# Kernel tuning notes

Measured on AMD Instinct MI355X. Metric: run time of the kernel, lower is better.

## Reference

```python
import jax, jax.numpy as jnp
import numpy as np

N_NODES = 100000


def spmm(edge_src, edge_dst, edge_val, x):
    """z[dst] += val * x[src] over all edges (COO sparse-dense matmul)."""
    gathered = edge_val[:, None] * x[edge_src]  # [E, d]
    return jax.ops.segment_sum(gathered, edge_dst, num_segments=N_NODES)


def setup_inputs() -> dict:
    key = jax.random.key(0)
    k1, k2, k3, k4, k5, k6 = jax.random.split(key, 6)
    N, E, IN, H, C = N_NODES, 1600000, 256, 128, 40
    features = jax.random.normal(k1, (N, IN), dtype=jnp.float32)
    # xavier_uniform-like init
    b1 = float(np.sqrt(6.0 / (IN + H)))
    b2 = float(np.sqrt(6.0 / (H + C)))
    W1 = jax.random.uniform(k2, (IN, H), dtype=jnp.float32, minval=-b1, maxval=b1)
    W2 = jax.random.uniform(k3, (H, C), dtype=jnp.float32, minval=-b2, maxval=b2)
    edge_src = jax.random.randint(k4, (E,), 0, N, dtype=jnp.int32)
    edge_dst = jnp.sort(jax.random.randint(k5, (E,), 0, N, dtype=jnp.int32))
    # normalized-adjacency-like positive edge weights
    edge_val = jax.random.uniform(k6, (E,), dtype=jnp.float32)
    return {"features": features, "W1": W1, "W2": W2,
            "edge_src": edge_src, "edge_dst": edge_dst, "edge_val": edge_val}


def reference(features, W1, W2, edge_src, edge_dst, edge_val):
    # Decoupled GCN: all dense NN layers first (relu between, none after last) ...
    h = jax.nn.relu(features @ W1)
    h = h @ W2  # [N, num_classes]
    # ... then nlayers (=2) rounds of graph propagation (spmm aggregation)
    h = spmm(edge_src, edge_dst, edge_val, h)
    h = spmm(edge_src, edge_dst, edge_val, h)
    return h
```

## Files before the change

kernel.cpp:

```cpp
#include <hip/hip_runtime.h>
#include <cstddef>
#include <cstdint>

#define IN_DIM 256
#define H_DIM  128
#define C_DIM  40
#define BM     128
#define BK     64
#define LDT    72
#define LDH    136
#define PAD_C  64

typedef short bf16x8 __attribute__((ext_vector_type(8)));
typedef float f32x16 __attribute__((ext_vector_type(16)));

__device__ __forceinline__ ushort f2bf(float f) {
  uint u = __builtin_bit_cast(uint, f);
  u += 0x7fffu + ((u >> 16) & 1u);
  return (ushort)(u >> 16);
}
__device__ __forceinline__ float bf2f(uint s) {
  uint u = s << 16;
  return __builtin_bit_cast(float, u);
}

__global__ void build_row_ptr_kernel(const int* __restrict__ dst, int E,
                                     int* __restrict__ row_ptr, int n1) {
  int n = blockIdx.x * blockDim.x + threadIdx.x;
  if (n >= n1) return;
  int lo = 0, hi = E;
  while (lo < hi) {
    int mid = (lo + hi) >> 1;
    if (dst[mid] < n) lo = mid + 1; else hi = mid;
  }
  row_ptr[n] = lo;
}

__global__ void convert_weights_kernel(const float* __restrict__ W1,
                                       const float* __restrict__ W2,
                                       ushort* __restrict__ w1t,
                                       ushort* __restrict__ w2t) {
  int tid = blockIdx.x * blockDim.x + threadIdx.x;
  if (tid < IN_DIM * H_DIM) {
    int k = tid >> 7, n = tid & 127;
    w1t[n * IN_DIM + k] = f2bf(W1[tid]);
  } else {
    int i = tid - IN_DIM * H_DIM;
    int n = i >> 7, k = i & 127;
    w2t[i] = (n < C_DIM) ? f2bf(W2[k * C_DIM + n]) : (ushort)0;
  }
}

__global__ __launch_bounds__(256, 3) void fused_dense_kernel(
    const float* __restrict__ feat, const ushort* __restrict__ w1t,
    const ushort* __restrict__ w2t, ushort* __restrict__ z0, int N) {
  __shared__ __align__(16) ushort smem[26112];

  const int t = threadIdx.x;
  const int w = t >> 6, l = t & 63;
  const int nb = blockIdx.x * BM;

  f32x16 acc[4];
#pragma unroll
  for (int tn = 0; tn < 4; ++tn)
#pragma unroll
    for (int r = 0; r < 16; ++r) acc[tn][r] = 0.f;

  const int srow = t >> 1;
  const int skh  = (t & 1) << 5;
  int grow = nb + srow; if (grow >= N) grow = N - 1;
  const float*  fp = feat + (size_t)grow * IN_DIM + skh;
  const ushort* wp = w1t + (srow << 8) + skh;

  const ushort* Abase = smem + (w * 32 + (l & 31)) * LDT + ((l >> 5) << 3);
  const ushort* Bbase = smem + 128 * LDT + (l & 31) * LDT + ((l >> 5) << 3);

  for (int kc = 0; kc < IN_DIM; kc += BK) {
    const float4* f4 = (const float4*)(fp + kc);
    uint* adst = (uint*)(smem + srow * LDT + skh);
#pragma unroll
    for (int i = 0; i < 4; ++i) {
      float4 v0 = f4[2 * i], v1 = f4[2 * i + 1];
      uint4 pk;
      pk.x = (uint)f2bf(v0.x) | ((uint)f2bf(v0.y) << 16);
      pk.y = (uint)f2bf(v0.z) | ((uint)f2bf(v0.w) << 16);
      pk.z = (uint)f2bf(v1.x) | ((uint)f2bf(v1.y) << 16);
      pk.w = (uint)f2bf(v1.z) | ((uint)f2bf(v1.w) << 16);
      ((uint4*)adst)[i] = pk;
    }
    const uint4* bsrc = (const uint4*)(wp + kc);
    uint4* bdst = (uint4*)(smem + 128 * LDT + srow * LDT + skh);
#pragma unroll
    for (int i = 0; i < 4; ++i) bdst[i] = bsrc[i];
    __syncthreads();

#pragma unroll
    for (int ks = 0; ks < 4; ++ks) {
      bf16x8 af = *(const bf16x8*)(Abase + ks * 16);
#pragma unroll
      for (int tn = 0; tn < 4; ++tn) {
        bf16x8 bfr = *(const bf16x8*)(Bbase + tn * 32 * LDT + ks * 16);
        acc[tn] = __builtin_amdgcn_mfma_f32_32x32x16_bf16(af, bfr, acc[tn], 0, 0, 0);
      }
    }
    __syncthreads();
  }

#pragma unroll
  for (int tn = 0; tn < 4; ++tn) {
    int col = tn * 32 + (l & 31);
#pragma unroll
    for (int r = 0; r < 16; ++r) {
      int nodeLoc = (r & 3) + 8 * (r >> 2) + 4 * (l >> 5) + 32 * w;
      float v = acc[tn][r];
      smem[nodeLoc * LDH + col] = f2bf(v > 0.f ? v : 0.f);
    }
  }
  {
    int row = t >> 2, c4 = (t & 3) << 5;
    const uint4* src = (const uint4*)(w2t + row * H_DIM + c4);
    uint4* dst = (uint4*)(smem + 128 * LDH + row * LDH + c4);
    dst[0] = src[0];
    dst[1] = src[1];
    dst[2] = src[2];
    dst[3] = src[3];
  }
  __syncthreads();

  f32x16 acc2[2];
#pragma unroll
  for (int tn = 0; tn < 2; ++tn)
#pragma unroll
    for (int r = 0; r < 16; ++r) acc2[tn][r] = 0.f;

  const ushort* Hbase  = smem + (w * 32 + (l & 31)) * LDH + ((l >> 5) << 3);
  const ushort* W2base = smem + 128 * LDH + (l & 31) * LDH + ((l >> 5) << 3);
#pragma unroll
  for (int kb = 0; kb < 8; ++kb) {
    bf16x8 af = *(const bf16x8*)(Hbase + kb * 16);
#pragma unroll
    for (int tn = 0; tn < 2; ++tn) {
      bf16x8 bfr = *(const bf16x8*)(W2base + tn * 32 * LDH + kb * 16);
      acc2[tn] = __builtin_amdgcn_mfma_f32_32x32x16_bf16(af, bfr, acc2[tn], 0, 0, 0);
    }
  }

#pragma unroll
  for (int tn = 0; tn < 2; ++tn) {
    int col = tn * 32 + (l & 31);
#pragma unroll
    for (int r = 0; r < 16; ++r) {
      int node = nb + 32 * w + (r & 3) + 8 * (r >> 2) + 4 * (l >> 5);
      if (node < N) z0[(size_t)node * PAD_C + col] = f2bf(acc2[tn][r]);
    }
  }
}

__global__ __launch_bounds__(256) void spmm_kernel(
    const int* __restrict__ row_ptr, const int* __restrict__ esrc,
    const float* __restrict__ eval, const ushort* __restrict__ x,
    ushort* __restrict__ zb, float* __restrict__ zf, int N, int out_f32) {
  int node = (blockIdx.x << 2) + (threadIdx.x >> 6);
  if (node >= N) return;
  const int lane = threadIdx.x & 63;
  const int h = lane >> 3;
  const int j = lane & 7;

  int e   = row_ptr[node];
  int end = row_ptr[node + 1];

  float acc[8];
#pragma unroll
  for (int c = 0; c < 8; ++c) acc[c] = 0.f;

  for (; e + 8 <= end; e += 8) {
    int   s = esrc[e + h];
    float v = eval[e + h];
    uint4 u = *(const uint4*)(x + (size_t)s * PAD_C + j * 8);
    acc[0] = fmaf(v, bf2f(u.x & 0xffffu), acc[0]);
    acc[1] = fmaf(v, bf2f(u.x >> 16),     acc[1]);
    acc[2] = fmaf(v, bf2f(u.y & 0xffffu), acc[2]);
    acc[3] = fmaf(v, bf2f(u.y >> 16),     acc[3]);
    acc[4] = fmaf(v, bf2f(u.z & 0xffffu), acc[4]);
    acc[5] = fmaf(v, bf2f(u.z >> 16),     acc[5]);
    acc[6] = fmaf(v, bf2f(u.w & 0xffffu), acc[6]);
    acc[7] = fmaf(v, bf2f(u.w >> 16),     acc[7]);
  }
  if (e < end) {
    int ei = e + h;
    int ec = ei < end - 1 ? ei : end - 1;
    int   s = esrc[ec];
    float v = (ei < end) ? eval[ec] : 0.f;
    uint4 u = *(const uint4*)(x + (size_t)s * PAD_C + j * 8);
    acc[0] = fmaf(v, bf2f(u.x & 0xffffu), acc[0]);
    acc[1] = fmaf(v, bf2f(u.x >> 16),     acc[1]);
    acc[2] = fmaf(v, bf2f(u.y & 0xffffu), acc[2]);
    acc[3] = fmaf(v, bf2f(u.y >> 16),     acc[3]);
    acc[4] = fmaf(v, bf2f(u.z & 0xffffu), acc[4]);
    acc[5] = fmaf(v, bf2f(u.z >> 16),     acc[5]);
    acc[6] = fmaf(v, bf2f(u.w & 0xffffu), acc[6]);
    acc[7] = fmaf(v, bf2f(u.w >> 16),     acc[7]);
  }

#pragma unroll
  for (int c = 0; c < 8; ++c) acc[c] += __shfl_xor(acc[c], 8);
#pragma unroll
  for (int c = 0; c < 8; ++c) acc[c] += __shfl_xor(acc[c], 16);
#pragma unroll
  for (int c = 0; c < 8; ++c) acc[c] += __shfl_xor(acc[c], 32);

  if (out_f32) {
    if (lane < 5) {
      float4 o0 = {acc[0], acc[1], acc[2], acc[3]};
      float4 o1 = {acc[4], acc[5], acc[6], acc[7]};
      float* p = zf + (size_t)node * C_DIM + j * 8;
      *(float4*)(p + 0) = o0;
      *(float4*)(p + 4) = o1;
    }
  } else {
    if (lane < 8) {
      uint4 p;
      p.x = (uint)f2bf(acc[0]) | ((uint)f2bf(acc[1]) << 16);
      p.y = (uint)f2bf(acc[2]) | ((uint)f2bf(acc[3]) << 16);
      p.z = (uint)f2bf(acc[4]) | ((uint)f2bf(acc[5]) << 16);
      p.w = (uint)f2bf(acc[6]) | ((uint)f2bf(acc[7]) << 16);
      *(uint4*)(zb + (size_t)node * PAD_C + j * 8) = p;
    }
  }
}

extern "C" void kernel_launch(void* const* d_in, const int* in_sizes, int n_in,
                              void* d_out, int out_size, void* d_ws, size_t ws_size,
                              hipStream_t stream) {
  const float* feat  = (const float*)d_in[0];
  const float* W1    = (const float*)d_in[1];
  const float* W2    = (const float*)d_in[2];
  const int*   esrc  = (const int*)d_in[3];
  const int*   edst  = (const int*)d_in[4];
  const float* evalp = (const float*)d_in[5];
  float* out = (float*)d_out;

  const int N = in_sizes[0] / IN_DIM;
  const int E = in_sizes[3];

  char* ws = (char*)d_ws;
  ushort* z0  = (ushort*)ws;
  ushort* z1  = (ushort*)(ws + (size_t)N * PAD_C * 2);
  ushort* w1t = (ushort*)(ws + (size_t)N * PAD_C * 4);
  ushort* w2t = w1t + IN_DIM * H_DIM;
  int* row_ptr = (int*)((char*)(w2t + PAD_C * H_DIM));

  build_row_ptr_kernel<<<(N + 256) / 256, 256, 0, stream>>>(edst, E, row_ptr, N + 1);
  convert_weights_kernel<<<(IN_DIM * H_DIM + PAD_C * H_DIM) / 256, 256, 0, stream>>>(
      W1, W2, w1t, w2t);
  fused_dense_kernel<<<(N + BM - 1) / BM, 256, 0, stream>>>(feat, w1t, w2t, z0, N);
  spmm_kernel<<<(N + 3) / 4, 256, 0, stream>>>(row_ptr, esrc, evalp, z0, z1, nullptr, N, 0);
  spmm_kernel<<<(N + 3) / 4, 256, 0, stream>>>(row_ptr, esrc, evalp, z1, nullptr, out, N, 1);
}
```

Before: 286.1 us.

## Prefetch dense-GEMM tiles in registers and process two nodes per wave in SpMM

The dense kernel now double-buffers its feature and weight tile loads in registers, loading chunk k+1 while chunk k is converted and multiplied, and uses nontemporal loads for the streamed features. The SpMM kernel maps two nodes per 64-lane wave, with 4 edges per iteration instead of 8, so that fewer lanes sit idle on the average degree of 16 and fewer reduction shuffles are needed. Edge arrays and row pointers are read with nontemporal hints. The trade-off is higher register pressure in the dense kernel and more loop iterations per node in SpMM.

Measured after the change: 318.3 us. 1.11x slower.

```diff
diff --git a/kernel.cpp b/kernel.cpp
--- a/kernel.cpp
+++ b/kernel.cpp
@@ -13,6 +13,8 @@
 
 typedef short bf16x8 __attribute__((ext_vector_type(8)));
 typedef float f32x16 __attribute__((ext_vector_type(16)));
+typedef float f32x4  __attribute__((ext_vector_type(4)));
+typedef uint  u32x4  __attribute__((ext_vector_type(4)));
 
 __device__ __forceinline__ ushort f2bf(float f) {
   uint u = __builtin_bit_cast(uint, f);
@@ -74,24 +76,40 @@
 
   const ushort* Abase = smem + (w * 32 + (l & 31)) * LDT + ((l >> 5) << 3);
   const ushort* Bbase = smem + 128 * LDT + (l & 31) * LDT + ((l >> 5) << 3);
-
-  for (int kc = 0; kc < IN_DIM; kc += BK) {
-    const float4* f4 = (const float4*)(fp + kc);
-    uint* adst = (uint*)(smem + srow * LDT + skh);
+  uint4* adst = (uint4*)(smem + srow * LDT + skh);
+  u32x4* bdst = (u32x4*)(smem + 128 * LDT + srow * LDT + skh);
+
+  f32x4 fa[2][8];
+  u32x4 wb[2][4];
+#pragma unroll
+  for (int i = 0; i < 8; ++i)
+    fa[0][i] = __builtin_nontemporal_load((const f32x4*)fp + i);
+#pragma unroll
+  for (int i = 0; i < 4; ++i) wb[0][i] = ((const u32x4*)wp)[i];
+
+#pragma unroll
+  for (int kc = 0; kc < 4; ++kc) {
+    const int cur = kc & 1, nxt = cur ^ 1;
+    if (kc < 3) {
+      const f32x4* fn = (const f32x4*)(fp + (kc + 1) * BK);
+      const u32x4* bn = (const u32x4*)(wp + (kc + 1) * BK);
+#pragma unroll
+      for (int i = 0; i < 8; ++i) fa[nxt][i] = __builtin_nontemporal_load(fn + i);
+#pragma unroll
+      for (int i = 0; i < 4; ++i) wb[nxt][i] = bn[i];
+    }
 #pragma unroll
     for (int i = 0; i < 4; ++i) {
-      float4 v0 = f4[2 * i], v1 = f4[2 * i + 1];
+      f32x4 v0 = fa[cur][2 * i], v1 = fa[cur][2 * i + 1];
       uint4 pk;
-      pk.x = (uint)f2bf(v0.x) | ((uint)f2bf(v0.y) << 16);
-      pk.y = (uint)f2bf(v0.z) | ((uint)f2bf(v0.w) << 16);
-      pk.z = (uint)f2bf(v1.x) | ((uint)f2bf(v1.y) << 16);
-      pk.w = (uint)f2bf(v1.z) | ((uint)f2bf(v1.w) << 16);
-      ((uint4*)adst)[i] = pk;
-    }
-    const uint4* bsrc = (const uint4*)(wp + kc);
-    uint4* bdst = (uint4*)(smem + 128 * LDT + srow * LDT + skh);
-#pragma unroll
-    for (int i = 0; i < 4; ++i) bdst[i] = bsrc[i];
+      pk.x = (uint)f2bf(v0[0]) | ((uint)f2bf(v0[1]) << 16);
+      pk.y = (uint)f2bf(v0[2]) | ((uint)f2bf(v0[3]) << 16);
+      pk.z = (uint)f2bf(v1[0]) | ((uint)f2bf(v1[1]) << 16);
+      pk.w = (uint)f2bf(v1[2]) | ((uint)f2bf(v1[3]) << 16);
+      adst[i] = pk;
+    }
+#pragma unroll
+    for (int i = 0; i < 4; ++i) bdst[i] = wb[cur][i];
     __syncthreads();
 
 #pragma unroll
@@ -160,23 +178,27 @@
     const int* __restrict__ row_ptr, const int* __restrict__ esrc,
     const float* __restrict__ eval, const ushort* __restrict__ x,
     ushort* __restrict__ zb, float* __restrict__ zf, int N, int out_f32) {
-  int node = (blockIdx.x << 2) + (threadIdx.x >> 6);
-  if (node >= N) return;
   const int lane = threadIdx.x & 63;
-  const int h = lane >> 3;
-  const int j = lane & 7;
-
-  int e   = row_ptr[node];
-  int end = row_ptr[node + 1];
+  const int wv   = threadIdx.x >> 6;
+  const int sub  = lane >> 5;
+  const int h    = (lane >> 3) & 3;
+  const int j    = lane & 7;
+
+  int node = blockIdx.x * 8 + wv * 2 + sub;
+  const bool valid = node < N;
+  if (!valid) node = N - 1;
+
+  int e   = __builtin_nontemporal_load(row_ptr + node);
+  int end = __builtin_nontemporal_load(row_ptr + node + 1);
 
   float acc[8];
 #pragma unroll
   for (int c = 0; c < 8; ++c) acc[c] = 0.f;
 
-  for (; e + 8 <= end; e += 8) {
-    int   s = esrc[e + h];
-    float v = eval[e + h];
-    uint4 u = *(const uint4*)(x + (size_t)s * PAD_C + j * 8);
+  for (; e + 4 <= end; e += 4) {
+    int   s = __builtin_nontemporal_load(esrc + e + h);
+    float v = __builtin_nontemporal_load(eval + e + h);
+    u32x4 u = *(const u32x4*)(x + (size_t)s * PAD_C + j * 8);
     acc[0] = fmaf(v, bf2f(u.x & 0xffffu), acc[0]);
     acc[1] = fmaf(v, bf2f(u.x >> 16),     acc[1]);
     acc[2] = fmaf(v, bf2f(u.y & 0xffffu), acc[2]);
@@ -188,10 +210,11 @@
   }
   if (e < end) {
     int ei = e + h;
-    int ec = ei < end - 1 ? ei : end - 1;
-    int   s = esrc[ec];
-    float v = (ei < end) ? eval[ec] : 0.f;
-    uint4 u = *(const uint4*)(x + (size_t)s * PAD_C + j * 8);
+    int ec = ei < end ? ei : end - 1;
+    int   s  = __builtin_nontemporal_load(esrc + ec);
+    float v0 = __builtin_nontemporal_load(eval + ec);
+    float v  = ei < end ? v0 : 0.f;
+    u32x4 u = *(const u32x4*)(x + (size_t)s * PAD_C + j * 8);
     acc[0] = fmaf(v, bf2f(u.x & 0xffffu), acc[0]);
     acc[1] = fmaf(v, bf2f(u.x >> 16),     acc[1]);
     acc[2] = fmaf(v, bf2f(u.y & 0xffffu), acc[2]);
@@ -206,19 +229,17 @@
   for (int c = 0; c < 8; ++c) acc[c] += __shfl_xor(acc[c], 8);
 #pragma unroll
   for (int c = 0; c < 8; ++c) acc[c] += __shfl_xor(acc[c], 16);
-#pragma unroll
-  for (int c = 0; c < 8; ++c) acc[c] += __shfl_xor(acc[c], 32);
-
-  if (out_f32) {
-    if (lane < 5) {
-      float4 o0 = {acc[0], acc[1], acc[2], acc[3]};
-      float4 o1 = {acc[4], acc[5], acc[6], acc[7]};
-      float* p = zf + (size_t)node * C_DIM + j * 8;
-      *(float4*)(p + 0) = o0;
-      *(float4*)(p + 4) = o1;
-    }
-  } else {
-    if (lane < 8) {
+
+  if (valid && h == 0) {
+    if (out_f32) {
+      if (j < 5) {
+        float4 o0 = {acc[0], acc[1], acc[2], acc[3]};
+        float4 o1 = {acc[4], acc[5], acc[6], acc[7]};
+        float* p = zf + (size_t)node * C_DIM + j * 8;
+        *(float4*)(p + 0) = o0;
+        *(float4*)(p + 4) = o1;
+      }
+    } else {
       uint4 p;
       p.x = (uint)f2bf(acc[0]) | ((uint)f2bf(acc[1]) << 16);
       p.y = (uint)f2bf(acc[2]) | ((uint)f2bf(acc[3]) << 16);
@@ -254,6 +275,6 @@
   convert_weights_kernel<<<(IN_DIM * H_DIM + PAD_C * H_DIM) / 256, 256, 0, stream>>>(
       W1, W2, w1t, w2t);
   fused_dense_kernel<<<(N + BM - 1) / BM, 256, 0, stream>>>(feat, w1t, w2t, z0, N);
-  spmm_kernel<<<(N + 3) / 4, 256, 0, stream>>>(row_ptr, esrc, evalp, z0, z1, nullptr, N, 0);
-  spmm_kernel<<<(N + 3) / 4, 256, 0, stream>>>(row_ptr, esrc, evalp, z1, nullptr, out, N, 1);
-}
+  spmm_kernel<<<(N + 7) / 8, 256, 0, stream>>>(row_ptr, esrc, evalp, z0, z1, nullptr, N, 0);
+  spmm_kernel<<<(N + 7) / 8, 256, 0, stream>>>(row_ptr, esrc, evalp, z1, nullptr, out, N, 1);
+}
```
